# Kernel optimization log

Measured on AMD Instinct MI355X. Metric: run time of the kernel, lower is better.

Reference implementation:

```python
import jax, jax.numpy as jnp
import numpy as np

BACKBONE_C = 480
NUM_SEG = 4
HIDDEN = 128
IN_DIM = 2 + BACKBONE_C + NUM_SEG + 2  # 488
N_NODES = 200000
N_EDGES = 800000
FH = FW = 128


def _bilinear_sample(feat, vertices, image_size):
    # feat: (C, H, W); vertices: (N, 2) in pixel space.
    # Matches F.grid_sample(..., mode='bilinear', align_corners=True) with
    # grid = vertices/image_size*2 - 1  =>  ix = vx/image_size*(W-1).
    C, H, W = feat.shape
    ix = vertices[:, 0] / image_size * (W - 1)
    iy = vertices[:, 1] / image_size * (H - 1)
    x0 = jnp.floor(ix)
    y0 = jnp.floor(iy)
    wx = ix - x0
    wy = iy - y0
    x0i = jnp.clip(x0.astype(jnp.int32), 0, W - 1)
    x1i = jnp.clip(x0i + 1, 0, W - 1)
    y0i = jnp.clip(y0.astype(jnp.int32), 0, H - 1)
    y1i = jnp.clip(y0i + 1, 0, H - 1)
    f00 = feat[:, y0i, x0i]  # (C, N)
    f01 = feat[:, y0i, x1i]
    f10 = feat[:, y1i, x0i]
    f11 = feat[:, y1i, x1i]
    out = (f00 * (1 - wx) * (1 - wy) + f01 * wx * (1 - wy)
           + f10 * (1 - wx) * wy + f11 * wx * wy)
    return out.T  # (N, C)


def setup_inputs() -> dict:
    key = jax.random.key(0)
    k = jax.random.split(key, 8)
    vertices = jax.random.uniform(k[0], (N_NODES, 2), jnp.float32) * 512.0
    backbone_features = jax.random.normal(k[1], (1, BACKBONE_C, FH, FW), jnp.float32)
    seg_probs = jax.random.uniform(k[2], (1, NUM_SEG, FH, FW), jnp.float32)
    edge_index = jax.random.randint(k[3], (2, N_EDGES), 0, N_NODES, jnp.int64)
    s1 = 1.0 / np.sqrt(IN_DIM)
    s2 = 1.0 / np.sqrt(HIDDEN)
    W1 = jax.random.uniform(k[4], (HIDDEN, IN_DIM), jnp.float32, -s1, s1)
    b1 = jax.random.uniform(k[5], (HIDDEN,), jnp.float32, -s1, s1)
    W2 = jax.random.uniform(k[6], (HIDDEN, HIDDEN), jnp.float32, -s2, s2)
    b2 = jax.random.uniform(k[7], (HIDDEN,), jnp.float32, -s2, s2)
    return {"vertices": vertices, "backbone_features": backbone_features,
            "seg_probs": seg_probs, "edge_index": edge_index,
            "W1": W1, "b1": b1, "W2": W2, "b2": b2, "image_size": 512}


def reference(vertices, backbone_features, seg_probs, edge_index, W1, b1, W2, b2, image_size):
    N = vertices.shape[0]
    coords_norm = vertices / image_size  # (N, 2)
    backbone_feats = _bilinear_sample(backbone_features[0], vertices, image_size)  # (N, C)
    seg_stats = _bilinear_sample(seg_probs[0], vertices, image_size)  # (N, num_seg)
    # degree via scatter-add over both endpoints
    idx = jnp.concatenate([edge_index[0], edge_index[1]]).astype(jnp.int32)
    degree = jax.ops.segment_sum(jnp.ones(idx.shape[0], jnp.float32), idx, num_segments=N)
    degree_norm = degree / (degree.max() + 1e-6)
    # distance to nearest image boundary, normalized by image_size/2
    dx = jnp.minimum(vertices[:, 0], image_size - vertices[:, 0])
    dy = jnp.minimum(vertices[:, 1], image_size - vertices[:, 1])
    dist_to_boundary = jnp.minimum(dx, dy) / (image_size / 2)
    structural = jnp.stack([degree_norm, dist_to_boundary], axis=1)  # (N, 2)
    node_feats = jnp.concatenate([coords_norm, backbone_feats, seg_stats, structural], axis=1)  # (N, 488)
    h = jax.nn.relu(node_feats @ W1.T + b1)
    h = jax.nn.relu(h @ W2.T + b2)
    return h
```

## Files before the change

kernel.cpp:

```cpp
#include <hip/hip_runtime.h>

typedef _Float16 half_t;
typedef __attribute__((ext_vector_type(2))) _Float16 halfx2;
typedef __attribute__((ext_vector_type(8))) _Float16 halfx8;
typedef __attribute__((ext_vector_type(4))) float floatx4;

#define N_NODES 200000
#define N_EDGES 800000
#define NPOS    16384
#define KIN     484

#define NSLICE  32
#define NRANGE  8
#define RNODES  25000
#define RWORDS  6250
#define CWORDS  50000
#define SCHUNK  12500

#define WS_DEGPK 0
#define WS_DEG   6400000
#define WS_MAXD  7200000
#define WS_W2H   7200064
#define WS_W1H   7232832
#define WS_U     7363904

__global__ __launch_bounds__(256) void k0(const float* __restrict__ W1,
                                          const float* __restrict__ W2,
                                          half_t* __restrict__ w2h,
                                          half_t* __restrict__ w1h) {
  const int tid = threadIdx.x, bid = blockIdx.x;
  if (bid == 0) {
    for (int i = tid; i < 128 * 128; i += 256) w2h[i] = (half_t)W2[i];
  } else {
    int j = bid - 1;
    const float* row = W1 + j * 488 + 2;
    int k1 = tid, k2 = tid + 256;
    w1h[j * 512 + k1] = (half_t)((k1 < KIN) ? row[k1] : 0.f);
    w1h[j * 512 + k2] = (half_t)((k2 < KIN) ? row[k2] : 0.f);
  }
}

__global__ __launch_bounds__(256) void k1(const half_t* __restrict__ w1h,
                                          const float* __restrict__ bb,
                                          const float* __restrict__ seg,
                                          const int* __restrict__ e,
                                          unsigned* __restrict__ degpk,
                                          half_t* __restrict__ U) {
  __shared__ __align__(16) char sm[25600];

  const int tid = threadIdx.x;
  const int bid = blockIdx.x;

  if (bid < 256) {
    half_t* Bl = (half_t*)sm;
    half_t* Ol = (half_t*)(sm + 5120);

    const int n0 = bid * 64;
    const int wave = tid >> 6, lane = tid & 63;
    const int l15 = lane & 15, q8 = (lane >> 4) * 8;

    floatx4 acc[2][4];
    for (int mt = 0; mt < 2; ++mt)
      for (int nt = 0; nt < 4; ++nt)
        acc[mt][nt] = (floatx4){0.f, 0.f, 0.f, 0.f};

    for (int kb = 0; kb < 512; kb += 32) {
      halfx8 af[2];
      for (int mt = 0; mt < 2; ++mt)
        af[mt] = *(const halfx8*)&w1h[(wave * 32 + mt * 16 + l15) * 512 + kb + q8];

      {
        int kk = tid >> 3, nc = (tid & 7) * 8;
        int k = kb + kk;
        float vals[8];
        if (k < 480) {
          const float* src = bb + k * NPOS + n0 + nc;
          float4 a = *(const float4*)(src);
          float4 b = *(const float4*)(src + 4);
          vals[0] = a.x; vals[1] = a.y; vals[2] = a.z; vals[3] = a.w;
          vals[4] = b.x; vals[5] = b.y; vals[6] = b.z; vals[7] = b.w;
        } else if (k < KIN) {
          const float* src = seg + (k - 480) * NPOS + n0 + nc;
          float4 a = *(const float4*)(src);
          float4 b = *(const float4*)(src + 4);
          vals[0] = a.x; vals[1] = a.y; vals[2] = a.z; vals[3] = a.w;
          vals[4] = b.x; vals[5] = b.y; vals[6] = b.z; vals[7] = b.w;
        } else {
          for (int i = 0; i < 8; ++i) vals[i] = 0.f;
        }
        for (int i = 0; i < 8; ++i) Bl[(nc + i) * 40 + kk] = (half_t)vals[i];
      }
      __syncthreads();

      halfx8 bf[4];
      for (int nt = 0; nt < 4; ++nt)
        bf[nt] = *(const halfx8*)&Bl[(nt * 16 + l15) * 40 + q8];
      for (int mt = 0; mt < 2; ++mt)
        for (int nt = 0; nt < 4; ++nt)
          acc[mt][nt] = __builtin_amdgcn_mfma_f32_16x16x32_f16(af[mt], bf[nt],
                                                               acc[mt][nt], 0, 0, 0);
      __syncthreads();
    }

    for (int mt = 0; mt < 2; ++mt)
      for (int nt = 0; nt < 4; ++nt)
        for (int r = 0; r < 4; ++r) {
          int j = wave * 32 + mt * 16 + (lane >> 4) * 4 + r;
          int n = nt * 16 + l15;
          Ol[n * 136 + j] = (half_t)acc[mt][nt][r];
        }
    __syncthreads();
    for (int it = 0; it < 4; ++it) {
      int idx = tid + it * 256;
      int n = idx >> 4, c8 = (idx & 15) * 8;
      *(halfx8*)(U + (long)(n0 + n) * 128 + c8) = *(const halfx8*)&Ol[n * 136 + c8];
    }
  } else {
    unsigned* cnt = (unsigned*)sm;
    const int hb = bid - 256;
    const int s  = hb >> 3;
    const int r  = hb & 7;
    const int lo = r * RNODES;
    const int lane = tid & 63;

    for (int i = tid; i < 64 + RWORDS; i += 256) cnt[i] = 0;
    __syncthreads();

#define HBIN(v) { unsigned d = (unsigned)(v) - (unsigned)lo;                 \
                  bool ok = d < (unsigned)RNODES;                            \
                  unsigned w = ok ? (d >> 2) + 64u : (unsigned)lane;         \
                  unsigned a_ = ok ? (1u << ((d & 3u) << 3)) : 0u;           \
                  atomicAdd(&cnt[w], a_); }

    const int4* E4 = (const int4*)e + s * SCHUNK;
    for (int base = 0; base < 12288; base += 1024) {
      int4 a = E4[base + tid];
      int4 b = E4[base + tid + 256];
      int4 c = E4[base + tid + 512];
      int4 d4 = E4[base + tid + 768];
      HBIN(a.x); HBIN(a.y); HBIN(a.z); HBIN(a.w);
      HBIN(b.x); HBIN(b.y); HBIN(b.z); HBIN(b.w);
      HBIN(c.x); HBIN(c.y); HBIN(c.z); HBIN(c.w);
      HBIN(d4.x); HBIN(d4.y); HBIN(d4.z); HBIN(d4.w);
    }
    if (tid < SCHUNK - 12288) {
      int4 a = E4[12288 + tid];
      HBIN(a.x); HBIN(a.y); HBIN(a.z); HBIN(a.w);
    }
#undef HBIN
    __syncthreads();

    unsigned* dst = degpk + s * CWORDS + r * RWORDS;
    for (int i = tid; i < RWORDS; i += 256) dst[i] = cnt[64 + i];
  }
}

__global__ __launch_bounds__(256) void k2(const unsigned* __restrict__ degpk,
                                          unsigned* __restrict__ deg,
                                          unsigned* __restrict__ maxd) {
  const int w4 = blockIdx.x * 256 + threadIdx.x;
  unsigned m = 0;
  if (w4 < CWORDS / 4) {
    uint4 s = make_uint4(0u, 0u, 0u, 0u);
    for (int c = 0; c < NSLICE; ++c) {
      uint4 v = *(const uint4*)&degpk[c * CWORDS + w4 * 4];
      s.x += v.x; s.y += v.y; s.z += v.z; s.w += v.w;
    }
    unsigned words[4] = {s.x, s.y, s.z, s.w};
    for (int k = 0; k < 4; ++k) {
      unsigned sw = words[k];
      uint4 o = make_uint4(sw & 255u, (sw >> 8) & 255u,
                           (sw >> 16) & 255u, sw >> 24);
      *(uint4*)&deg[w4 * 16 + k * 4] = o;
      m = max(m, max(max(o.x, o.y), max(o.z, o.w)));
    }
  }
  for (int off = 32; off > 0; off >>= 1) {
    unsigned o = (unsigned)__shfl_down((int)m, off);
    m = max(m, o);
  }
  if ((threadIdx.x & 63) == 0) atomicMax(maxd, m);
}

__global__ __launch_bounds__(256) void k_main(const float* __restrict__ vertices,
                                              const float* __restrict__ W1,
                                              const float* __restrict__ b1,
                                              const float* __restrict__ b2,
                                              const unsigned* __restrict__ deg,
                                              const unsigned* __restrict__ maxd,
                                              const half_t* __restrict__ U,
                                              const half_t* __restrict__ w2h,
                                              float* __restrict__ out) {
  __shared__ half_t At[64 * 136];
  __shared__ half_t W2l[128 * 72];
  __shared__ int   pPos[64];
  __shared__ float pW[4][64];
  __shared__ float pE[4][64];
  __shared__ float b2l[128];

  const int tid = threadIdx.x;
  const int nodeBase = blockIdx.x * 64;

  if (tid < 128) b2l[tid] = b2[tid];

  if (tid < 64) {
    int n = nodeBase + tid;
    float vx = vertices[2 * n], vy = vertices[2 * n + 1];
    float ix = vx * (127.0f / 512.0f), iy = vy * (127.0f / 512.0f);
    float fx = floorf(ix), fy = floorf(iy);
    float wx = ix - fx, wy = iy - fy;
    int x0 = min(max((int)fx, 0), 127);
    int y0 = min(max((int)fy, 0), 127);
    pPos[tid] = y0 * 128 + x0;
    pW[0][tid] = (1.f - wx) * (1.f - wy);
    pW[1][tid] = wx * (1.f - wy);
    pW[2][tid] = (1.f - wx) * wy;
    pW[3][tid] = wx * wy;
    pE[0][tid] = vx * (1.f / 512.f);
    pE[1][tid] = vy * (1.f / 512.f);
    float md = (float)(*maxd) + 1e-6f;
    pE[2][tid] = (float)deg[n] / md;
    float dx = fminf(vx, 512.f - vx), dy = fminf(vy, 512.f - vy);
    pE[3][tid] = fminf(dx, dy) * (1.f / 256.f);
  }

  const int jp = tid & 63, q = tid >> 6;
  const int j2 = jp * 2;
  const float* r0 = W1 + j2 * 488;
  const float* r1 = r0 + 488;
  float c00 = r0[0], c01 = r0[1], c06 = r0[486], c07 = r0[487];
  float c10 = r1[0], c11 = r1[1], c16 = r1[486], c17 = r1[487];
  float bb0 = b1[j2], bb1 = b1[j2 + 1];
  __syncthreads();

  for (int it = 0; it < 16; ++it) {
    int ln = it * 4 + q;
    int pos = pPos[ln];
    float w00 = pW[0][ln], w01 = pW[1][ln], w10 = pW[2][ln], w11 = pW[3][ln];
    float cx = pE[0][ln], cy = pE[1][ln], dn = pE[2][ln], db = pE[3][ln];
    const half_t* base = U + (long)pos * 128 + j2;
    halfx2 u00 = *(const halfx2*)(base);
    halfx2 u01 = *(const halfx2*)(base + 128);
    halfx2 u10 = *(const halfx2*)(base + 16384);
    halfx2 u11 = *(const halfx2*)(base + 16512);
    float z0 = bb0 + c00 * cx + c01 * cy + c06 * dn + c07 * db
             + w00 * (float)u00.x + w01 * (float)u01.x
             + w10 * (float)u10.x + w11 * (float)u11.x;
    float z1 = bb1 + c10 * cx + c11 * cy + c16 * dn + c17 * db
             + w00 * (float)u00.y + w01 * (float)u01.y
             + w10 * (float)u10.y + w11 * (float)u11.y;
    halfx2 h;
    h.x = (half_t)fmaxf(z0, 0.f);
    h.y = (half_t)fmaxf(z1, 0.f);
    *(halfx2*)&At[ln * 136 + j2] = h;
  }
  __syncthreads();

  const int wave = tid >> 6, lane = tid & 63;
  const int l15 = lane & 15, q4 = lane >> 4;
  floatx4 acc[8];
  for (int t = 0; t < 8; ++t) acc[t] = (floatx4){0.f, 0.f, 0.f, 0.f};

  for (int h = 0; h < 2; ++h) {
    __syncthreads();
    for (int it = 0; it < 4; ++it) {
      int idx = tid + it * 256;
      int r = idx >> 3, c8 = (idx & 7) * 8;
      *(halfx8*)&W2l[r * 72 + c8] = *(const halfx8*)&w2h[r * 128 + h * 64 + c8];
    }
    __syncthreads();
    for (int ks = 0; ks < 64; ks += 32) {
      halfx8 af = *(const halfx8*)&At[(wave * 16 + l15) * 136 + h * 64 + ks + q4 * 8];
      for (int t = 0; t < 8; ++t) {
        halfx8 bf = *(const halfx8*)&W2l[(t * 16 + l15) * 72 + ks + q4 * 8];
        acc[t] = __builtin_amdgcn_mfma_f32_16x16x32_f16(af, bf, acc[t], 0, 0, 0);
      }
    }
  }

  for (int t = 0; t < 8; ++t) {
    int col = t * 16 + l15;
    float bias = b2l[col];
    int row0 = nodeBase + wave * 16 + q4 * 4;
    for (int r = 0; r < 4; ++r)
      out[(long)(row0 + r) * 128 + col] = fmaxf(acc[t][r] + bias, 0.f);
  }
}

extern "C" void kernel_launch(void* const* d_in, const int* in_sizes, int n_in,
                              void* d_out, int out_size, void* d_ws, size_t ws_size,
                              hipStream_t stream) {
  const float* vertices = (const float*)d_in[0];
  const float* bb       = (const float*)d_in[1];
  const float* seg      = (const float*)d_in[2];
  const int*   edges    = (const int*)d_in[3];
  const float* W1       = (const float*)d_in[4];
  const float* b1       = (const float*)d_in[5];
  const float* W2       = (const float*)d_in[6];
  const float* b2       = (const float*)d_in[7];

  char* ws = (char*)d_ws;
  unsigned* degpk = (unsigned*)(ws + WS_DEGPK);
  unsigned* deg   = (unsigned*)(ws + WS_DEG);
  unsigned* maxd  = (unsigned*)(ws + WS_MAXD);
  half_t*   w2h   = (half_t*)(ws + WS_W2H);
  half_t*   w1h   = (half_t*)(ws + WS_W1H);
  half_t*   U     = (half_t*)(ws + WS_U);
  float*    outp  = (float*)d_out;

  hipMemsetAsync(ws + WS_MAXD, 0, 64, stream);
  k0<<<129, 256, 0, stream>>>(W1, W2, w2h, w1h);
  k1<<<256 + NSLICE * NRANGE, 256, 0, stream>>>(w1h, bb, seg, edges, degpk, U);
  k2<<<49, 256, 0, stream>>>(degpk, deg, maxd);
  k_main<<<3125, 256, 0, stream>>>(vertices, W1, b1, b2, deg, maxd, U, w2h, outp);
}
```

Before: 231.9 us.

## Pre-swizzle W2 into MFMA fragment order and read it directly from global

W2 is now converted in k0 into a layout matching the MFMA B-fragment order. k_main then loads B fragments straight from global/L2 with contiguous 16-byte reads instead of staging W2 through LDS. This removes the W2 LDS buffer and two barriers per half, which cuts LDS use and should allow more blocks per CU. A launch-bounds occupancy hint and a partial unroll of the gather loop are added too. The cost is repeated per-wave global loads of W2, which rely on cache hits.

Measured after the change: 214.2 us. -7.7%, faster.

```diff
diff --git a/kernel.cpp b/kernel.cpp
--- a/kernel.cpp
+++ b/kernel.cpp
@@ -20,17 +20,27 @@
 #define WS_DEGPK 0
 #define WS_DEG   6400000
 #define WS_MAXD  7200000
-#define WS_W2H   7200064
+#define WS_W2F   7200064
 #define WS_W1H   7232832
 #define WS_U     7363904
 
 __global__ __launch_bounds__(256) void k0(const float* __restrict__ W1,
                                           const float* __restrict__ W2,
-                                          half_t* __restrict__ w2h,
+                                          half_t* __restrict__ w2f,
                                           half_t* __restrict__ w1h) {
   const int tid = threadIdx.x, bid = blockIdx.x;
   if (bid == 0) {
-    for (int i = tid; i < 128 * 128; i += 256) w2h[i] = (half_t)W2[i];
+    for (int i = tid; i < 128 * 128; i += 256) {
+      int k8   = i & 7;
+      int l15  = (i >> 3) & 15;
+      int q4   = (i >> 7) & 3;
+      int ks32 = (i >> 9) & 1;
+      int h    = (i >> 10) & 1;
+      int t    = i >> 11;
+      int row = t * 16 + l15;
+      int col = h * 64 + ks32 * 32 + q4 * 8 + k8;
+      w2f[i] = (half_t)W2[row * 128 + col];
+    }
   } else {
     int j = bid - 1;
     const float* row = W1 + j * 488 + 2;
@@ -182,17 +192,16 @@
   if ((threadIdx.x & 63) == 0) atomicMax(maxd, m);
 }
 
-__global__ __launch_bounds__(256) void k_main(const float* __restrict__ vertices,
+__global__ __launch_bounds__(256, 8) void k_main(const float* __restrict__ vertices,
                                               const float* __restrict__ W1,
                                               const float* __restrict__ b1,
                                               const float* __restrict__ b2,
                                               const unsigned* __restrict__ deg,
                                               const unsigned* __restrict__ maxd,
                                               const half_t* __restrict__ U,
-                                              const half_t* __restrict__ w2h,
+                                              const half_t* __restrict__ w2f,
                                               float* __restrict__ out) {
   __shared__ half_t At[64 * 136];
-  __shared__ half_t W2l[128 * 72];
   __shared__ int   pPos[64];
   __shared__ float pW[4][64];
   __shared__ float pE[4][64];
@@ -233,6 +242,7 @@
   float bb0 = b1[j2], bb1 = b1[j2 + 1];
   __syncthreads();
 
+#pragma unroll 4
   for (int it = 0; it < 16; ++it) {
     int ln = it * 4 + q;
     int pos = pPos[ln];
@@ -258,25 +268,19 @@
 
   const int wave = tid >> 6, lane = tid & 63;
   const int l15 = lane & 15, q4 = lane >> 4;
+  const half_t* wf = w2f + (q4 * 16 + l15) * 8;
   floatx4 acc[8];
   for (int t = 0; t < 8; ++t) acc[t] = (floatx4){0.f, 0.f, 0.f, 0.f};
 
-  for (int h = 0; h < 2; ++h) {
-    __syncthreads();
-    for (int it = 0; it < 4; ++it) {
-      int idx = tid + it * 256;
-      int r = idx >> 3, c8 = (idx & 7) * 8;
-      *(halfx8*)&W2l[r * 72 + c8] = *(const halfx8*)&w2h[r * 128 + h * 64 + c8];
-    }
-    __syncthreads();
-    for (int ks = 0; ks < 64; ks += 32) {
-      halfx8 af = *(const halfx8*)&At[(wave * 16 + l15) * 136 + h * 64 + ks + q4 * 8];
+  for (int h = 0; h < 2; ++h)
+    for (int ks32 = 0; ks32 < 2; ++ks32) {
+      halfx8 af = *(const halfx8*)&At[(wave * 16 + l15) * 136 + h * 64 +
+                                      ks32 * 32 + q4 * 8];
       for (int t = 0; t < 8; ++t) {
-        halfx8 bf = *(const halfx8*)&W2l[(t * 16 + l15) * 72 + ks + q4 * 8];
+        halfx8 bf = *(const halfx8*)&wf[(t * 4 + h * 2 + ks32) * 512];
         acc[t] = __builtin_amdgcn_mfma_f32_16x16x32_f16(af, bf, acc[t], 0, 0, 0);
       }
     }
-  }
 
   for (int t = 0; t < 8; ++t) {
     int col = t * 16 + l15;
@@ -303,14 +307,14 @@
   unsigned* degpk = (unsigned*)(ws + WS_DEGPK);
   unsigned* deg   = (unsigned*)(ws + WS_DEG);
   unsigned* maxd  = (unsigned*)(ws + WS_MAXD);
-  half_t*   w2h   = (half_t*)(ws + WS_W2H);
+  half_t*   w2f   = (half_t*)(ws + WS_W2F);
   half_t*   w1h   = (half_t*)(ws + WS_W1H);
   half_t*   U     = (half_t*)(ws + WS_U);
   float*    outp  = (float*)d_out;
 
   hipMemsetAsync(ws + WS_MAXD, 0, 64, stream);
-  k0<<<129, 256, 0, stream>>>(W1, W2, w2h, w1h);
+  k0<<<129, 256, 0, stream>>>(W1, W2, w2f, w1h);
   k1<<<256 + NSLICE * NRANGE, 256, 0, stream>>>(w1h, bb, seg, edges, degpk, U);
   k2<<<49, 256, 0, stream>>>(degpk, deg, maxd);
-  k_main<<<3125, 256, 0, stream>>>(vertices, W1, b1, b2, deg, maxd, U, w2h, outp);
-}
+  k_main<<<3125, 256, 0, stream>>>(vertices, W1, b1, b2, deg, maxd, U, w2f, outp);
+}
```
